# Kernel tuning notes

Hardware: AMD Instinct MI355X
Metric: run time of the kernel (lower is better)

## Reference

```python
import jax, jax.numpy as jnp
import numpy as np
import math

L_LAYERS = 4
EMBED = 512
HEADS = 8
FFN = 2048
EPS = 1e-20
PAD_IDX = 0


def sinusoidal_table(num_embeddings, embedding_dim, padding_idx=0):
    half = embedding_dim // 2
    freq = jnp.exp(jnp.arange(half, dtype=jnp.float32) * (-math.log(10000.0) / (half - 1)))
    ang = jnp.arange(num_embeddings, dtype=jnp.float32)[:, None] * freq[None, :]
    emb = jnp.concatenate([jnp.sin(ang), jnp.cos(ang)], axis=1)
    if padding_idx is not None:
        emb = emb.at[padding_idx].set(0.0)
    return emb  # [num_embeddings, embedding_dim]


def layer_norm(x, g, b):
    mu = jnp.mean(x, axis=-1, keepdims=True)
    var = jnp.mean((x - mu) ** 2, axis=-1, keepdims=True)
    return (x - mu) * jax.lax.rsqrt(var + EPS) * g + b


def mha(x_q, x_kv, Wqkv, bqkv, Wo, bo, mask):
    """Custom attention: scaled scores, multiplicative mask, GLOBAL min-max norm (no softmax)."""
    T, B, C = x_q.shape
    S = x_kv.shape[0]
    hd = C // HEADS
    scale = hd ** -0.5
    q = x_q @ Wqkv[:C].T + bqkv[:C]
    k = x_kv @ Wqkv[C:2 * C].T + bqkv[C:2 * C]
    v = x_kv @ Wqkv[2 * C:].T + bqkv[2 * C:]
    q = q * scale
    # [T,B,C] -> [B*H, T, hd]
    q = q.reshape(T, B * HEADS, hd).transpose(1, 0, 2)
    k = k.reshape(S, B * HEADS, hd).transpose(1, 0, 2)
    v = v.reshape(S, B * HEADS, hd).transpose(1, 0, 2)
    w = jnp.einsum('bth,bsh->bts', q, k)  # [B*H, T, S]
    if mask is not None:
        w = w * mask[None, :, :]
    # global min-max normalization (as in the torch source)
    w = (w - jnp.min(w)) / (jnp.max(w) - jnp.min(w))
    a = jnp.einsum('bts,bsh->bth', w, v)  # [B*H, T, hd]
    a = a.transpose(1, 0, 2).reshape(T, B, C)
    return a @ Wo.T + bo


def setup_inputs() -> dict:
    key = jax.random.key(0)
    ks = iter(jax.random.split(key, 32))
    T, B, C, F, L = 2048, 2, EMBED, FFN, L_LAYERS
    d = {}
    d['x'] = jax.random.normal(next(ks), (T, B, C), dtype=jnp.float32)
    d['enc_out'] = jax.random.normal(next(ks), (T, B, C), dtype=jnp.float32)
    d['tokens'] = jax.random.randint(next(ks), (B, T), 0, 32000, dtype=jnp.int64 if jax.config.read('jax_enable_x64') else jnp.int32)
    sd = C ** -0.5
    d['self_Wqkv'] = jax.random.normal(next(ks), (L, 3 * C, C)) * sd
    d['self_bqkv'] = jnp.zeros((L, 3 * C))
    d['self_Wo'] = jax.random.normal(next(ks), (L, C, C)) * sd
    d['self_bo'] = jnp.zeros((L, C))
    d['cross_Wqkv'] = jax.random.normal(next(ks), (L, 3 * C, C)) * sd
    d['cross_bqkv'] = jnp.zeros((L, 3 * C))
    d['cross_Wo'] = jax.random.normal(next(ks), (L, C, C)) * sd
    d['cross_bo'] = jnp.zeros((L, C))
    d['fc1_w'] = jax.random.normal(next(ks), (L, F, C)) * sd
    d['fc1_b'] = jnp.zeros((L, F))
    d['fc2_w'] = jax.random.normal(next(ks), (L, C, F)) * (F ** -0.5)
    d['fc2_b'] = jnp.zeros((L, C))
    d['ln1_g'] = jnp.ones((L, C)); d['ln1_b'] = jnp.zeros((L, C))
    d['ln2_g'] = jnp.ones((L, C)); d['ln2_b'] = jnp.zeros((L, C))
    d['ln3_g'] = jnp.ones((L, C)); d['ln3_b'] = jnp.zeros((L, C))
    return d


def _forward(x, enc_out, tokens, self_Wqkv, self_bqkv, self_Wo, self_bo,
             cross_Wqkv, cross_bqkv, cross_Wo, cross_bo,
             fc1_w, fc1_b, fc2_w, fc2_b, ln1_g, ln1_b, ln2_g, ln2_b, ln3_g, ln3_b):
    T, B, C = x.shape
    # sinusoidal positional embedding (make_positions with padding_idx=0, no left pad)
    table = sinusoidal_table(PAD_IDX + 1 + T, C, PAD_IDX)
    pos = jnp.where(tokens != PAD_IDX, jnp.arange(1, T + 1)[None, :], 0)  # [B, T]
    pe = table[pos]  # [B, T, C]
    x = x + pe.transpose(1, 0, 2)
    # multiplicative future mask: tril of ones
    fmask = jnp.tril(jnp.ones((T, T), dtype=x.dtype))
    for l in range(L_LAYERS):
        # self-attention
        res = x
        x = mha(x, x, self_Wqkv[l], self_bqkv[l], self_Wo[l], self_bo[l], fmask)
        x = layer_norm(res + x, ln1_g[l], ln1_b[l])
        # cross-attention (no mask)
        res = x
        x = mha(x, enc_out, cross_Wqkv[l], cross_bqkv[l], cross_Wo[l], cross_bo[l], None)
        x = layer_norm(res + x, ln2_g[l], ln2_b[l])
        # FFN
        res = x
        h = jax.nn.relu(x @ fc1_w[l].T + fc1_b[l])
        x = h @ fc2_w[l].T + fc2_b[l]
        x = layer_norm(res + x, ln3_g[l], ln3_b[l])
    return x


def reference(x, enc_out, tokens, self_Wqkv, self_bqkv, self_Wo, self_bo,
              cross_Wqkv, cross_bqkv, cross_Wo, cross_bo,
              fc1_w, fc1_b, fc2_w, fc2_b, ln1_g, ln1_b, ln2_g, ln2_b, ln3_g, ln3_b):
    return _forward(x, enc_out, tokens, self_Wqkv, self_bqkv, self_Wo, self_bo,
                    cross_Wqkv, cross_bqkv, cross_Wo, cross_bo,
                    fc1_w, fc1_b, fc2_w, fc2_b, ln1_g, ln1_b, ln2_g, ln2_b, ln3_g, ln3_b)
```

## Files before the change

kernel.cpp:

```cpp
#include <hip/hip_runtime.h>
#include <math.h>

typedef __bf16 bf16;
typedef unsigned short u16;
typedef __bf16 bf16x8 __attribute__((ext_vector_type(8)));
typedef float f32x4 __attribute__((ext_vector_type(4)));

#define T_SEQ 2048
#define NB    2
#define CE    512
#define NH    8
#define HD    64
#define ROWS  4096
#define NBH   16
#define LDT   40
#define LDA   72

#define MFMA16(a,b,c) __builtin_amdgcn_mfma_f32_16x16x32_bf16((a),(b),(c),0,0,0)

__global__ __launch_bounds__(256) void sniff(const u16* __restrict__ xs,
                                             const int* __restrict__ toks,
                                             int* __restrict__ flags)
{
  const int tid = threadIdx.x;
  int crazy = 0, ze = 0;
  for (int i = tid; i < 4096; i += 256) {
    int e = (xs[i] >> 7) & 0xFF;
    if (e >= 141) crazy++;
    if (((i & 1) == 0) && (xs[i] == 0)) ze++;
  }
  int zc = 0;
  for (int i = tid; i < 1024; i += 256)
    if (toks[2 * i + 1] == 0) zc++;
  __shared__ int r1[4], r2[4], r3[4];
#pragma unroll
  for (int o = 32; o; o >>= 1) {
    crazy += __shfl_down(crazy, o); ze += __shfl_down(ze, o); zc += __shfl_down(zc, o);
  }
  if ((tid & 63) == 0) { r1[tid >> 6] = crazy; r2[tid >> 6] = ze; r3[tid >> 6] = zc; }
  __syncthreads();
  if (tid == 0) {
    int c = r1[0] + r1[1] + r1[2] + r1[3];
    int z = r2[0] + r2[1] + r2[2] + r2[3];
    int t = r3[0] + r3[1] + r3[2] + r3[3];
    flags[0] = (z > 1500 || c > 64) ? 1 : 0;
    flags[1] = (t > 900) ? 1 : 0;
  }
}

static __device__ __forceinline__ float ldf(const void* src, size_t eoff, bool f32) {
  return f32 ? ((const float*)src)[eoff] : (float)((const bf16*)src)[eoff];
}

__global__ __launch_bounds__(256) void posembed(const void* __restrict__ xsrc,
                                                const int* __restrict__ toks,
                                                const int* __restrict__ flags,
                                                float* __restrict__ xf)
{
  const bool f32 = flags[0] != 0;
  const bool tok64 = flags[1] != 0;
  const int row = blockIdx.x;
  const int t = row >> 1, b = row & 1;
  const int tix = b * T_SEQ + t;
  const int tok = tok64 ? toks[2 * tix] : toks[tix];
  const int p = (tok != 0) ? (t + 1) : 0;
  const float kf = -0.0361193740f;
  for (int c = threadIdx.x; c < CE; c += 256) {
    float pe = 0.0f;
    if (p != 0) {
      int i = (c < 256) ? c : (c - 256);
      float freq = expf((float)i * kf);
      float ang = (float)p * freq;
      pe = (c < 256) ? sinf(ang) : cosf(ang);
    }
    xf[(size_t)row * CE + c] = ldf(xsrc, (size_t)row * CE + c, f32) + pe;
  }
}

template<bool RELUF, bool AFFINE>
__global__ __launch_bounds__(256) void gemm_mfma(const void* __restrict__ A, int a_inp,
                                                 const void* __restrict__ Bw, size_t bwOff,
                                                 const void* __restrict__ bias, size_t biasOff,
                                                 const int* __restrict__ flags,
                                                 float* __restrict__ Cf,
                                                 int M, int N, int K, int kspan,
                                                 long long partStride,
                                                 const float* __restrict__ mmf,
                                                 const float* __restrict__ vsum)
{
  __shared__ __align__(16) bf16 Ah[128 * LDT];
  __shared__ __align__(16) bf16 Al[128 * LDT];
  __shared__ __align__(16) bf16 Bh[128 * LDT];
  __shared__ __align__(16) bf16 Bl[128 * LDT];
  const int fl = flags[0];
  const bool a_f32 = (a_inp == 0) ? true : (fl != 0);
  const bool b_f32 = (fl != 0);
  const int tid = threadIdx.x;
  const int m0 = blockIdx.y * 128, n0 = blockIdx.x * 128;
  const int srow = tid >> 1;
  const int skc  = (tid & 1) * 16;
  const int wid = tid >> 6, lane = tid & 63;
  const int wm = (wid >> 1) * 64, wn = (wid & 1) * 64;
  const int fr = lane & 15;
  const int fk = (lane >> 4) * 8;
  const int kb = blockIdx.z * kspan;
  const int ke = (kb + kspan < K) ? (kb + kspan) : K;
  float* Cp = Cf + (long long)blockIdx.z * partStride;
  const int arow1 = (m0 + srow) & 1;
  float inv_ = 0.0f, cmn_ = 0.0f;
  if (AFFINE) { inv_ = 1.0f / (mmf[1] - mmf[0]); cmn_ = mmf[0] * inv_; }
  f32x4 acc[4][4] = {};

  uint4 ra[4], rb[4];
  auto loadA = [&](int k0) {
    size_t g = (size_t)(m0 + srow) * K + k0 + skc;
    if (a_f32) {
      const uint4* p = (const uint4*)((const float*)A + g);
      ra[0] = p[0]; ra[1] = p[1]; ra[2] = p[2]; ra[3] = p[3];
    } else {
      const uint4* p = (const uint4*)((const bf16*)A + g);
      ra[0] = p[0]; ra[1] = p[1];
    }
  };
  auto loadB = [&](int k0) {
    size_t g = bwOff + (size_t)(n0 + srow) * K + k0 + skc;
    if (b_f32) {
      const uint4* p = (const uint4*)((const float*)Bw + g);
      rb[0] = p[0]; rb[1] = p[1]; rb[2] = p[2]; rb[3] = p[3];
    } else {
      const uint4* p = (const uint4*)((const bf16*)Bw + g);
      rb[0] = p[0]; rb[1] = p[1];
    }
  };
  auto cvtStore = [&](const uint4* r, bool f32src, bool wantLo, bf16* Hs, bf16* Ls) {
    float v[16];
    if (f32src) {
      const float* f = (const float*)r;
#pragma unroll
      for (int q = 0; q < 16; q++) v[q] = f[q];
    } else {
      const bf16* c = (const bf16*)r;
#pragma unroll
      for (int q = 0; q < 16; q++) v[q] = (float)c[q];
    }
    bf16x8 h0, h1, l0, l1;
#pragma unroll
    for (int q = 0; q < 8; q++) {
      bf16 ha = (bf16)v[q], hb = (bf16)v[8 + q];
      h0[q] = ha; h1[q] = hb;
      l0[q] = (bf16)(v[q]     - (float)ha);
      l1[q] = (bf16)(v[8 + q] - (float)hb);
    }
    *(bf16x8*)&Hs[srow * LDT + skc]     = h0;
    *(bf16x8*)&Hs[srow * LDT + skc + 8] = h1;
    if (wantLo) {
      *(bf16x8*)&Ls[srow * LDT + skc]     = l0;
      *(bf16x8*)&Ls[srow * LDT + skc + 8] = l1;
    }
  };

  loadA(kb); loadB(kb);
  for (int k0 = kb; k0 < ke; k0 += 32) {
    __syncthreads();
    if (AFFINE) {
      float* f = (float*)ra;
      const float* vs = vsum + arow1 * 512 + k0 + skc;
#pragma unroll
      for (int q = 0; q < 16; q++) f[q] = inv_ * f[q] - cmn_ * vs[q];
    }
    cvtStore(ra, a_f32, a_f32, Ah, Al);
    cvtStore(rb, b_f32, b_f32, Bh, Bl);
    __syncthreads();
    if (k0 + 32 < ke) { loadA(k0 + 32); loadB(k0 + 32); }
    bf16x8 ah[4], bh[4];
#pragma unroll
    for (int i = 0; i < 4; i++) ah[i] = *(const bf16x8*)&Ah[(wm + i*16 + fr) * LDT + fk];
#pragma unroll
    for (int j = 0; j < 4; j++) bh[j] = *(const bf16x8*)&Bh[(wn + j*16 + fr) * LDT + fk];
#pragma unroll
    for (int i = 0; i < 4; i++)
#pragma unroll
      for (int j = 0; j < 4; j++)
        acc[i][j] = MFMA16(ah[i], bh[j], acc[i][j]);
    if (a_f32) {
      bf16x8 al[4];
#pragma unroll
      for (int i = 0; i < 4; i++) al[i] = *(const bf16x8*)&Al[(wm + i*16 + fr) * LDT + fk];
#pragma unroll
      for (int i = 0; i < 4; i++)
#pragma unroll
        for (int j = 0; j < 4; j++)
          acc[i][j] = MFMA16(al[i], bh[j], acc[i][j]);
    }
    if (b_f32) {
      bf16x8 bl[4];
#pragma unroll
      for (int j = 0; j < 4; j++) bl[j] = *(const bf16x8*)&Bl[(wn + j*16 + fr) * LDT + fk];
#pragma unroll
      for (int i = 0; i < 4; i++)
#pragma unroll
        for (int j = 0; j < 4; j++)
          acc[i][j] = MFMA16(ah[i], bl[j], acc[i][j]);
    }
  }
  const int orow0 = m0 + wm + (lane >> 4) * 4;
  const int ocol0 = n0 + wn + (lane & 15);
  const bool addb = (blockIdx.z == 0);
#pragma unroll
  for (int j = 0; j < 4; j++) {
    int col = ocol0 + j * 16;
    float bv = addb ? ldf(bias, biasOff + col, b_f32) : 0.0f;
#pragma unroll
    for (int i = 0; i < 4; i++) {
#pragma unroll
      for (int r = 0; r < 4; r++) {
        float vv = acc[i][j][r] + bv;
        if (RELUF) vv = fmaxf(vv, 0.0f);
        Cp[(size_t)(orow0 + i * 16 + r) * N + col] = vv;
      }
    }
  }
}

__global__ __launch_bounds__(256) void prep_kv(const float* __restrict__ base, int ld,
                                               int kofs0, int vofs0,
                                               bf16* __restrict__ kh, bf16* __restrict__ kl,
                                               bf16* __restrict__ vth, bf16* __restrict__ vtl,
                                               float* __restrict__ vcs)
{
  __shared__ float ts[64 * 65];
  const int bh = blockIdx.x, s0 = blockIdx.y * 64;
  const int b = bh >> 3, h = bh & 7;
  const int kofs = kofs0 + h * HD, vofs = vofs0 + h * HD;
  const int tid = threadIdx.x;
#pragma unroll
  for (int it = 0; it < 16; ++it) {
    int idx = it * 256 + tid, r = idx >> 6, d = idx & 63;
    size_t rowb = (size_t)((s0 + r) * NB + b) * ld;
    float v = base[rowb + kofs + d];
    bf16 hi = (bf16)v;
    size_t o = ((size_t)bh * T_SEQ + s0 + r) * 64 + d;
    kh[o] = hi; kl[o] = (bf16)(v - (float)hi);
    ts[r * 65 + d] = base[rowb + vofs + d];
  }
  __syncthreads();
  const int d = tid >> 2, sseg = (tid & 3) * 16;
  bf16x8 hv0, lv0, hv1, lv1;
#pragma unroll
  for (int q = 0; q < 8; ++q) {
    float v0 = ts[(sseg + q) * 65 + d];
    float v1 = ts[(sseg + 8 + q) * 65 + d];
    bf16 h0 = (bf16)v0, h1 = (bf16)v1;
    hv0[q] = h0; lv0[q] = (bf16)(v0 - (float)h0);
    hv1[q] = h1; lv1[q] = (bf16)(v1 - (float)h1);
  }
  size_t o = ((size_t)bh * 64 + d) * T_SEQ + s0 + sseg;
  *(bf16x8*)&vth[o]     = hv0;
  *(bf16x8*)&vth[o + 8] = hv1;
  *(bf16x8*)&vtl[o]     = lv0;
  *(bf16x8*)&vtl[o + 8] = lv1;
  if (tid < 64) {
    float s = 0.0f;
    for (int j = 0; j < 64; ++j) s += ts[j * 65 + tid];
    vcs[((size_t)bh * 32 + blockIdx.y) * 64 + tid] = s;
  }
}

__device__ __forceinline__ int remap_ty(int ty) { return (ty < 16) ? ty : 47 - ty; }

template<bool MASK>
__global__ __launch_bounds__(256) void fattn(const float* __restrict__ qbase, int qld, int qofs0,
                                             const bf16* __restrict__ kh, const bf16* __restrict__ kl,
                                             const bf16* __restrict__ vth, const bf16* __restrict__ vtl,
                                             float* __restrict__ partial,
                                             float* __restrict__ pvout)
{
  __shared__ __align__(16) bf16 Qh[64 * LDA], Ql[64 * LDA];
  __shared__ __align__(16) bf16 Kh[64 * LDA], Kl[64 * LDA];
  __shared__ __align__(16) bf16 Vh[64 * LDA], Vl[64 * LDA];
  __shared__ __align__(16) bf16 Ph[64 * LDA], Pl[64 * LDA];
  __shared__ float rn[4], rx[4];
  const int bh = blockIdx.x, tyr = remap_ty(blockIdx.y);
  const int t0 = tyr * 64;
  const int b = bh >> 3, h = bh & 7;
  const int qofs = qofs0 + h * HD;
  const int tid = threadIdx.x;
#pragma unroll
  for (int it = 0; it < 16; ++it) {
    int idx = it * 256 + tid, r = idx >> 6, d = idx & 63;
    float v = qbase[(size_t)((t0 + r) * NB + b) * qld + qofs + d] * 0.125f;
    bf16 hi = (bf16)v;
    Qh[r * LDA + d] = hi; Ql[r * LDA + d] = (bf16)(v - (float)hi);
  }
  const int wid = tid >> 6, lane = tid & 63;
  const int wm_ = (wid >> 1) * 32, wn_ = (wid & 1) * 32;
  const int fr = lane & 15, fko = (lane >> 4) * 8;
  const int crr = (lane >> 4) * 4, crc = lane & 15;
  const int cr = tid >> 2, cseg = (tid & 3) * 16;
  float mn = 1e30f, mx = -1e30f;
  f32x4 o4[2][2] = {};
  const int nch = MASK ? (tyr + 1) : 32;
  for (int sc = 0; sc < nch; ++sc) {
    const int s0 = sc * 64;
    __syncthreads();
    {
      size_t go = ((size_t)bh * T_SEQ + s0 + cr) * 64 + cseg;
      *(bf16x8*)&Kh[cr * LDA + cseg]     = *(const bf16x8*)&kh[go];
      *(bf16x8*)&Kh[cr * LDA + cseg + 8] = *(const bf16x8*)&kh[go + 8];
      *(bf16x8*)&Kl[cr * LDA + cseg]     = *(const bf16x8*)&kl[go];
      *(bf16x8*)&Kl[cr * LDA + cseg + 8] = *(const bf16x8*)&kl[go + 8];
      size_t gv = ((size_t)bh * 64 + cr) * T_SEQ + s0 + cseg;
      *(bf16x8*)&Vh[cr * LDA + cseg]     = *(const bf16x8*)&vth[gv];
      *(bf16x8*)&Vh[cr * LDA + cseg + 8] = *(const bf16x8*)&vth[gv + 8];
      *(bf16x8*)&Vl[cr * LDA + cseg]     = *(const bf16x8*)&vtl[gv];
      *(bf16x8*)&Vl[cr * LDA + cseg + 8] = *(const bf16x8*)&vtl[gv + 8];
    }
    __syncthreads();
    f32x4 a4[2][2] = {};
#pragma unroll
    for (int ks = 0; ks < 2; ++ks) {
      bf16x8 aH[2], aL[2], bH[2], bL[2];
#pragma unroll
      for (int i = 0; i < 2; ++i) {
        aH[i] = *(const bf16x8*)&Qh[(wm_ + i*16 + fr) * LDA + ks*32 + fko];
        aL[i] = *(const bf16x8*)&Ql[(wm_ + i*16 + fr) * LDA + ks*32 + fko];
        bH[i] = *(const bf16x8*)&Kh[(wn_ + i*16 + fr) * LDA + ks*32 + fko];
        bL[i] = *(const bf16x8*)&Kl[(wn_ + i*16 + fr) * LDA + ks*32 + fko];
      }
#pragma unroll
      for (int i = 0; i < 2; ++i)
#pragma unroll
        for (int j = 0; j < 2; ++j) {
          a4[i][j] = MFMA16(aH[i], bH[j], a4[i][j]);
          a4[i][j] = MFMA16(aL[i], bH[j], a4[i][j]);
          a4[i][j] = MFMA16(aH[i], bL[j], a4[i][j]);
        }
    }
#pragma unroll
    for (int i = 0; i < 2; ++i)
#pragma unroll
      for (int j = 0; j < 2; ++j)
#pragma unroll
        for (int r = 0; r < 4; ++r) {
          int tl = wm_ + i*16 + crr + r;
          int sl = wn_ + j*16 + crc;
          float w = a4[i][j][r];
          if (MASK && (s0 + sl) > (t0 + tl)) w = 0.0f;
          mn = fminf(mn, w); mx = fmaxf(mx, w);
          bf16 wh = (bf16)w;
          Ph[tl * LDA + sl] = wh;
          Pl[tl * LDA + sl] = (bf16)(w - (float)wh);
        }
    __syncthreads();
#pragma unroll
    for (int ks = 0; ks < 2; ++ks) {
      bf16x8 pH[2], pL[2], vH[2], vL[2];
#pragma unroll
      for (int i = 0; i < 2; ++i) {
        pH[i] = *(const bf16x8*)&Ph[(wm_ + i*16 + fr) * LDA + ks*32 + fko];
        pL[i] = *(const bf16x8*)&Pl[(wm_ + i*16 + fr) * LDA + ks*32 + fko];
        vH[i] = *(const bf16x8*)&Vh[(wn_ + i*16 + fr) * LDA + ks*32 + fko];
        vL[i] = *(const bf16x8*)&Vl[(wn_ + i*16 + fr) * LDA + ks*32 + fko];
      }
#pragma unroll
      for (int i = 0; i < 2; ++i)
#pragma unroll
        for (int j = 0; j < 2; ++j) {
          o4[i][j] = MFMA16(pH[i], vH[j], o4[i][j]);
          o4[i][j] = MFMA16(pL[i], vH[j], o4[i][j]);
          o4[i][j] = MFMA16(pH[i], vL[j], o4[i][j]);
        }
    }
  }
#pragma unroll
  for (int i = 0; i < 2; ++i)
#pragma unroll
    for (int j = 0; j < 2; ++j)
#pragma unroll
      for (int r = 0; r < 4; ++r) {
        int tl = wm_ + i*16 + crr + r;
        int dl = wn_ + j*16 + crc;
        pvout[(size_t)((t0 + tl) * NB + b) * CE + h * HD + dl] = o4[i][j][r];
      }
#pragma unroll
  for (int o = 32; o; o >>= 1) { mn = fminf(mn, __shfl_down(mn, o)); mx = fmaxf(mx, __shfl_down(mx, o)); }
  if (lane == 0) { rn[wid] = mn; rx[wid] = mx; }
  __syncthreads();
  if (tid == 0) {
    int bidx = blockIdx.y * NBH + blockIdx.x;
    partial[2 * bidx]     = fminf(fminf(rn[0], rn[1]), fminf(rn[2], rn[3]));
    partial[2 * bidx + 1] = fmaxf(fmaxf(rx[0], rx[1]), fmaxf(rx[2], rx[3]));
  }
}

__global__ __launch_bounds__(512) void reduce_mm(const float* __restrict__ partial,
                                                 const float* __restrict__ vcs,
                                                 float* __restrict__ mmf,
                                                 float* __restrict__ vsum)
{
  const int tid = threadIdx.x, w = tid >> 6, l = tid & 63;
  __shared__ float rn[8], rx[8];
  float mn = partial[2 * tid], mx = partial[2 * tid + 1];
#pragma unroll
  for (int o = 32; o; o >>= 1) { mn = fminf(mn, __shfl_down(mn, o)); mx = fmaxf(mx, __shfl_down(mx, o)); }
  if (l == 0) { rn[w] = mn; rx[w] = mx; }
  __syncthreads();
  if (tid == 0) {
    float a = 1e30f, c = -1e30f;
#pragma unroll
    for (int i = 0; i < 8; i++) { a = fminf(a, rn[i]); c = fmaxf(c, rx[i]); }
    mmf[0] = a; mmf[1] = c;
  }
  for (int e = tid; e < 1024; e += 512) {
    int bh = e >> 6, d = e & 63;
    float s = 0.0f;
#pragma unroll
    for (int ch = 0; ch < 32; ++ch) s += vcs[(size_t)bh * 2048 + ch * 64 + d];
    vsum[e] = s;
  }
}

template<int NP>
__global__ __launch_bounds__(256) void ln_sum(const float* __restrict__ res,
                                              const float* __restrict__ p, long long pstride,
                                              const void* __restrict__ g, const void* __restrict__ be,
                                              size_t goff, const int* __restrict__ flags,
                                              float* __restrict__ xfo)
{
  __shared__ float red[4];
  const bool fl = flags[0] != 0;
  const int tid = threadIdx.x;
  const size_t base = (size_t)blockIdx.x * CE;
  float a  = res[base + tid];
  float b2 = res[base + tid + 256];
#pragma unroll
  for (int k = 0; k < NP; k++) {
    a  += p[(long long)k * pstride + base + tid];
    b2 += p[(long long)k * pstride + base + tid + 256];
  }
  float s = a + b2;
#pragma unroll
  for (int o = 32; o; o >>= 1) s += __shfl_down(s, o);
  if ((tid & 63) == 0) red[tid >> 6] = s;
  __syncthreads();
  float mu = (red[0] + red[1] + red[2] + red[3]) * (1.0f / 512.0f);
  __syncthreads();
  float da = a - mu, db = b2 - mu;
  float q = da * da + db * db;
#pragma unroll
  for (int o = 32; o; o >>= 1) q += __shfl_down(q, o);
  if ((tid & 63) == 0) red[tid >> 6] = q;
  __syncthreads();
  float var = (red[0] + red[1] + red[2] + red[3]) * (1.0f / 512.0f);
  float rs = rsqrtf(var + 1e-20f);
  xfo[base + tid]       = da * rs * ldf(g, goff + tid, fl)       + ldf(be, goff + tid, fl);
  xfo[base + tid + 256] = db * rs * ldf(g, goff + tid + 256, fl) + ldf(be, goff + tid + 256, fl);
}

extern "C" void kernel_launch(void* const* d_in, const int* in_sizes, int n_in,
                              void* d_out, int out_size, void* d_ws, size_t ws_size,
                              hipStream_t stream)
{
  (void)in_sizes; (void)n_in; (void)out_size; (void)ws_size;
  const void* x_in   = d_in[0];
  const void* enc_in = d_in[1];
  const int*  tokens = (const int*)d_in[2];
  const void* sWqkv = d_in[3];
  const void* sbqkv = d_in[4];
  const void* sWo   = d_in[5];
  const void* sbo   = d_in[6];
  const void* cWqkv = d_in[7];
  const void* cbqkv = d_in[8];
  const void* cWo   = d_in[9];
  const void* cbo   = d_in[10];
  const void* fc1w  = d_in[11];
  const void* fc1b  = d_in[12];
  const void* fc2w  = d_in[13];
  const void* fc2b  = d_in[14];
  const void* ln1g  = d_in[15];
  const void* ln1b  = d_in[16];
  const void* ln2g  = d_in[17];
  const void* ln2b  = d_in[18];
  const void* ln3g  = d_in[19];
  const void* ln3b  = d_in[20];

  char* ws = (char*)d_ws;
  size_t off = 0;
  auto alloc = [&](size_t bytes) -> char* {
    char* p = ws + off;
    off += (bytes + 255) & ~(size_t)255;
    return p;
  };
  int*   flags   = (int*)  alloc(256);
  float* mmf     = (float*)alloc(256);
  float* vsum    = (float*)alloc(1024 * 4);
  float* partial = (float*)alloc(4096);
  float* xf      = (float*)alloc((size_t)ROWS * CE * 4);
  float* y       = (float*)alloc((size_t)ROWS * CE * 4);
  float* qkv     = (float*)alloc((size_t)ROWS * 2048 * 4);
  float* pblk    = (float*)alloc((size_t)ROWS * CE * 4 * 4);
  bf16*  khb     = (bf16*) alloc((size_t)16 * T_SEQ * 64 * 2);
  bf16*  klb     = (bf16*) alloc((size_t)16 * T_SEQ * 64 * 2);
  bf16*  vth     = (bf16*) alloc((size_t)16 * 64 * T_SEQ * 2);
  bf16*  vtl     = (bf16*) alloc((size_t)16 * 64 * T_SEQ * 2);
  float* vcs     = (float*)alloc((size_t)16 * 32 * 64 * 4);
  float* kvb = qkv + (size_t)ROWS * 512;
  const long long PS_FULL = (long long)ROWS * CE;

  sniff<<<1, 256, 0, stream>>>((const u16*)x_in, tokens, flags);
  posembed<<<ROWS, 256, 0, stream>>>(x_in, tokens, flags, xf);

  for (int l = 0; l < 4; l++) {
    gemm_mfma<false, false><<<dim3(12, 32, 1), 256, 0, stream>>>(
        xf, 0, sWqkv, (size_t)l * 1536 * 512, sbqkv, (size_t)l * 1536, flags, qkv,
        ROWS, 1536, 512, 512, 0, nullptr, nullptr);
    prep_kv<<<dim3(16, 32), 256, 0, stream>>>(qkv, 1536, 512, 1024, khb, klb, vth, vtl, vcs);
    fattn<true><<<dim3(NBH, 32), 256, 0, stream>>>(qkv, 1536, 0, khb, klb, vth, vtl, partial, y);
    reduce_mm<<<1, 512, 0, stream>>>(partial, vcs, mmf, vsum);
    gemm_mfma<false, true><<<dim3(4, 32, 4), 256, 0, stream>>>(
        y, 0, sWo, (size_t)l * 512 * 512, sbo, (size_t)l * 512, flags, pblk,
        ROWS, 512, 512, 128, PS_FULL, mmf, vsum);
    ln_sum<4><<<ROWS, 256, 0, stream>>>(xf, pblk, PS_FULL, ln1g, ln1b, (size_t)l * 512, flags, xf);

    gemm_mfma<false, false><<<dim3(4, 32, 1), 256, 0, stream>>>(
        xf, 0, cWqkv, (size_t)l * 1536 * 512, cbqkv, (size_t)l * 1536, flags, qkv,
        ROWS, 512, 512, 512, 0, nullptr, nullptr);
    gemm_mfma<false, false><<<dim3(8, 32, 1), 256, 0, stream>>>(
        enc_in, 1, cWqkv, (size_t)l * 1536 * 512 + (size_t)512 * 512, cbqkv, (size_t)l * 1536 + 512,
        flags, kvb, ROWS, 1024, 512, 512, 0, nullptr, nullptr);
    prep_kv<<<dim3(16, 32), 256, 0, stream>>>(kvb, 1024, 0, 512, khb, klb, vth, vtl, vcs);
    fattn<false><<<dim3(NBH, 32), 256, 0, stream>>>(qkv, 512, 0, khb, klb, vth, vtl, partial, y);
    reduce_mm<<<1, 512, 0, stream>>>(partial, vcs, mmf, vsum);
    gemm_mfma<false, true><<<dim3(4, 32, 4), 256, 0, stream>>>(
        y, 0, cWo, (size_t)l * 512 * 512, cbo, (size_t)l * 512, flags, pblk,
        ROWS, 512, 512, 128, PS_FULL, mmf, vsum);
    ln_sum<4><<<ROWS, 256, 0, stream>>>(xf, pblk, PS_FULL, ln2g, ln2b, (size_t)l * 512, flags, xf);

    gemm_mfma<true, false><<<dim3(16, 32, 1), 256, 0, stream>>>(
        xf, 0, fc1w, (size_t)l * 2048 * 512, fc1b, (size_t)l * 2048, flags, qkv,
        ROWS, 2048, 512, 512, 0, nullptr, nullptr);
    gemm_mfma<false, false><<<dim3(4, 32, 4), 256, 0, stream>>>(
        qkv, 0, fc2w, (size_t)l * 512 * 2048, fc2b, (size_t)l * 512, flags, pblk,
        ROWS, 512, 2048, 512, PS_FULL, nullptr, nullptr);
    float* lnout = (l == 3) ? (float*)d_out : xf;
    ln_sum<4><<<ROWS, 256, 0, stream>>>(xf, pblk, PS_FULL, ln3g, ln3b, (size_t)l * 512, flags, lnout);
  }
}
```

Before: 2.777 ms.

## Double-buffer GEMM LDS tiles, swizzle blocks across XCDs, merge cross-attn QKV GEMMs

The GEMM kernel now keeps two LDS stages, so the next k-tile is converted and stored while the current one feeds the MFMAs, which removes one barrier per iteration. GEMM and attention launches use a 1D grid remapped so neighbouring tiles share an XCD and can reuse L2. The cross-attention Q projection (from xf) and the KV projection (from enc_out) now run as one launch, with column tiles choosing their A source. The cost is twice the LDS use, which may lower occupancy.

```diff
diff --git a/kernel.cpp b/kernel.cpp
--- a/kernel.cpp
+++ b/kernel.cpp
@@ -17,6 +17,12 @@
 #define LDA   72
 
 #define MFMA16(a,b,c) __builtin_amdgcn_mfma_f32_16x16x32_bf16((a),(b),(c),0,0,0)
+
+static __device__ __forceinline__ int xcd_swz(int id, int n) {
+  int q = n >> 3, r = n & 7;
+  int x = id & 7, o = id >> 3;
+  return (x < r) ? (x * (q + 1) + o) : (r * (q + 1) + (x - r) * q + o);
+}
 
 __global__ __launch_bounds__(256) void sniff(const u16* __restrict__ xs,
                                              const int* __restrict__ toks,
@@ -78,34 +84,44 @@
 }
 
 template<bool RELUF, bool AFFINE>
-__global__ __launch_bounds__(256) void gemm_mfma(const void* __restrict__ A, int a_inp,
+__global__ __launch_bounds__(256) void gemm_mfma(const float* __restrict__ A,
+                                                 const void* __restrict__ A2,
                                                  const void* __restrict__ Bw, size_t bwOff,
                                                  const void* __restrict__ bias, size_t biasOff,
                                                  const int* __restrict__ flags,
                                                  float* __restrict__ Cf,
-                                                 int M, int N, int K, int kspan,
+                                                 int N, int K, int kspan,
+                                                 int nbx, int nbxA,
                                                  long long partStride,
                                                  const float* __restrict__ mmf,
                                                  const float* __restrict__ vsum)
 {
-  __shared__ __align__(16) bf16 Ah[128 * LDT];
-  __shared__ __align__(16) bf16 Al[128 * LDT];
-  __shared__ __align__(16) bf16 Bh[128 * LDT];
-  __shared__ __align__(16) bf16 Bl[128 * LDT];
+  __shared__ __align__(16) bf16 AhS[2][128 * LDT];
+  __shared__ __align__(16) bf16 AlS[2][128 * LDT];
+  __shared__ __align__(16) bf16 BhS[2][128 * LDT];
+  __shared__ __align__(16) bf16 BlS[2][128 * LDT];
   const int fl = flags[0];
-  const bool a_f32 = (a_inp == 0) ? true : (fl != 0);
+  const int nblk = nbx * (int)1;
+  (void)nblk;
+  const int id = xcd_swz((int)blockIdx.x, (int)gridDim.x);
+  const int per_z = nbx * 32;
+  const int zz = id / per_z;
+  const int rem = id - zz * per_z;
+  const int by = rem / nbx, bx = rem - by * nbx;
+  const bool a_f32 = (bx < nbxA) ? true : (fl != 0);
+  const void* Abase = (bx < nbxA) ? (const void*)A : A2;
   const bool b_f32 = (fl != 0);
   const int tid = threadIdx.x;
-  const int m0 = blockIdx.y * 128, n0 = blockIdx.x * 128;
+  const int m0 = by * 128, n0 = bx * 128;
   const int srow = tid >> 1;
   const int skc  = (tid & 1) * 16;
   const int wid = tid >> 6, lane = tid & 63;
   const int wm = (wid >> 1) * 64, wn = (wid & 1) * 64;
   const int fr = lane & 15;
   const int fk = (lane >> 4) * 8;
-  const int kb = blockIdx.z * kspan;
+  const int kb = zz * kspan;
   const int ke = (kb + kspan < K) ? (kb + kspan) : K;
-  float* Cp = Cf + (long long)blockIdx.z * partStride;
+  float* Cp = Cf + (long long)zz * partStride;
   const int arow1 = (m0 + srow) & 1;
   float inv_ = 0.0f, cmn_ = 0.0f;
   if (AFFINE) { inv_ = 1.0f / (mmf[1] - mmf[0]); cmn_ = mmf[0] * inv_; }
@@ -115,10 +131,10 @@
   auto loadA = [&](int k0) {
     size_t g = (size_t)(m0 + srow) * K + k0 + skc;
     if (a_f32) {
-      const uint4* p = (const uint4*)((const float*)A + g);
+      const uint4* p = (const uint4*)((const float*)Abase + g);
       ra[0] = p[0]; ra[1] = p[1]; ra[2] = p[2]; ra[3] = p[3];
     } else {
-      const uint4* p = (const uint4*)((const bf16*)A + g);
+      const uint4* p = (const uint4*)((const bf16*)Abase + g);
       ra[0] = p[0]; ra[1] = p[1];
     }
   };
@@ -132,6 +148,14 @@
       rb[0] = p[0]; rb[1] = p[1];
     }
   };
+  auto fixA = [&](int k0) {
+    if (AFFINE) {
+      float* f = (float*)ra;
+      const float* vs = vsum + arow1 * 512 + k0 + skc;
+#pragma unroll
+      for (int q = 0; q < 16; q++) f[q] = inv_ * f[q] - cmn_ * vs[q];
+    }
+  };
   auto cvtStore = [&](const uint4* r, bool f32src, bool wantLo, bf16* Hs, bf16* Ls) {
     float v[16];
     if (f32src) {
@@ -160,23 +184,27 @@
   };
 
   loadA(kb); loadB(kb);
+  fixA(kb);
+  cvtStore(ra, a_f32, a_f32, AhS[0], AlS[0]);
+  cvtStore(rb, b_f32, b_f32, BhS[0], BlS[0]);
+  if (kb + 32 < ke) { loadA(kb + 32); loadB(kb + 32); }
+
+  int cur = 0;
   for (int k0 = kb; k0 < ke; k0 += 32) {
     __syncthreads();
-    if (AFFINE) {
-      float* f = (float*)ra;
-      const float* vs = vsum + arow1 * 512 + k0 + skc;
-#pragma unroll
-      for (int q = 0; q < 16; q++) f[q] = inv_ * f[q] - cmn_ * vs[q];
-    }
-    cvtStore(ra, a_f32, a_f32, Ah, Al);
-    cvtStore(rb, b_f32, b_f32, Bh, Bl);
-    __syncthreads();
-    if (k0 + 32 < ke) { loadA(k0 + 32); loadB(k0 + 32); }
+    if (k0 + 32 < ke) {
+      fixA(k0 + 32);
+      cvtStore(ra, a_f32, a_f32, AhS[cur ^ 1], AlS[cur ^ 1]);
+      cvtStore(rb, b_f32, b_f32, BhS[cur ^ 1], BlS[cur ^ 1]);
+      if (k0 + 64 < ke) { loadA(k0 + 64); loadB(k0 + 64); }
+    }
+    const bf16* Ahc = AhS[cur]; const bf16* Alc = AlS[cur];
+    const bf16* Bhc = BhS[cur]; const bf16* Blc = BlS[cur];
     bf16x8 ah[4], bh[4];
 #pragma unroll
-    for (int i = 0; i < 4; i++) ah[i] = *(const bf16x8*)&Ah[(wm + i*16 + fr) * LDT + fk];
-#pragma unroll
-    for (int j = 0; j < 4; j++) bh[j] = *(const bf16x8*)&Bh[(wn + j*16 + fr) * LDT + fk];
+    for (int i = 0; i < 4; i++) ah[i] = *(const bf16x8*)&Ahc[(wm + i*16 + fr) * LDT + fk];
+#pragma unroll
+    for (int j = 0; j < 4; j++) bh[j] = *(const bf16x8*)&Bhc[(wn + j*16 + fr) * LDT + fk];
 #pragma unroll
     for (int i = 0; i < 4; i++)
 #pragma unroll
@@ -185,7 +213,7 @@
     if (a_f32) {
       bf16x8 al[4];
 #pragma unroll
-      for (int i = 0; i < 4; i++) al[i] = *(const bf16x8*)&Al[(wm + i*16 + fr) * LDT + fk];
+      for (int i = 0; i < 4; i++) al[i] = *(const bf16x8*)&Alc[(wm + i*16 + fr) * LDT + fk];
 #pragma unroll
       for (int i = 0; i < 4; i++)
 #pragma unroll
@@ -195,17 +223,18 @@
     if (b_f32) {
       bf16x8 bl[4];
 #pragma unroll
-      for (int j = 0; j < 4; j++) bl[j] = *(const bf16x8*)&Bl[(wn + j*16 + fr) * LDT + fk];
+      for (int j = 0; j < 4; j++) bl[j] = *(const bf16x8*)&Blc[(wn + j*16 + fr) * LDT + fk];
 #pragma unroll
       for (int i = 0; i < 4; i++)
 #pragma unroll
         for (int j = 0; j < 4; j++)
           acc[i][j] = MFMA16(ah[i], bl[j], acc[i][j]);
     }
+    cur ^= 1;
   }
   const int orow0 = m0 + wm + (lane >> 4) * 4;
   const int ocol0 = n0 + wn + (lane & 15);
-  const bool addb = (blockIdx.z == 0);
+  const bool addb = (zz == 0);
 #pragma unroll
   for (int j = 0; j < 4; j++) {
     int col = ocol0 + j * 16;
@@ -280,7 +309,9 @@
   __shared__ __align__(16) bf16 Vh[64 * LDA], Vl[64 * LDA];
   __shared__ __align__(16) bf16 Ph[64 * LDA], Pl[64 * LDA];
   __shared__ float rn[4], rx[4];
-  const int bh = blockIdx.x, tyr = remap_ty(blockIdx.y);
+  const int id = xcd_swz((int)blockIdx.x, 512);
+  const int bh = id >> 5;
+  const int tyr = remap_ty(id & 31);
   const int t0 = tyr * 64;
   const int b = bh >> 3, h = bh & 7;
   const int qofs = qofs0 + h * HD;
@@ -387,9 +418,8 @@
   if (lane == 0) { rn[wid] = mn; rx[wid] = mx; }
   __syncthreads();
   if (tid == 0) {
-    int bidx = blockIdx.y * NBH + blockIdx.x;
-    partial[2 * bidx]     = fminf(fminf(rn[0], rn[1]), fminf(rn[2], rn[3]));
-    partial[2 * bidx + 1] = fmaxf(fmaxf(rx[0], rx[1]), fmaxf(rx[2], rx[3]));
+    partial[2 * id]     = fminf(fminf(rn[0], rn[1]), fminf(rn[2], rn[3]));
+    partial[2 * id + 1] = fmaxf(fmaxf(rx[0], rx[1]), fmaxf(rx[2], rx[3]));
   }
 }
 
@@ -504,44 +534,40 @@
   bf16*  vth     = (bf16*) alloc((size_t)16 * 64 * T_SEQ * 2);
   bf16*  vtl     = (bf16*) alloc((size_t)16 * 64 * T_SEQ * 2);
   float* vcs     = (float*)alloc((size_t)16 * 32 * 64 * 4);
-  float* kvb = qkv + (size_t)ROWS * 512;
   const long long PS_FULL = (long long)ROWS * CE;
 
   sniff<<<1, 256, 0, stream>>>((const u16*)x_in, tokens, flags);
   posembed<<<ROWS, 256, 0, stream>>>(x_in, tokens, flags, xf);
 
   for (int l = 0; l < 4; l++) {
-    gemm_mfma<false, false><<<dim3(12, 32, 1), 256, 0, stream>>>(
-        xf, 0, sWqkv, (size_t)l * 1536 * 512, sbqkv, (size_t)l * 1536, flags, qkv,
-        ROWS, 1536, 512, 512, 0, nullptr, nullptr);
+    gemm_mfma<false, false><<<384, 256, 0, stream>>>(
+        xf, xf, sWqkv, (size_t)l * 1536 * 512, sbqkv, (size_t)l * 1536, flags, qkv,
+        1536, 512, 512, 12, 12, 0, nullptr, nullptr);
     prep_kv<<<dim3(16, 32), 256, 0, stream>>>(qkv, 1536, 512, 1024, khb, klb, vth, vtl, vcs);
-    fattn<true><<<dim3(NBH, 32), 256, 0, stream>>>(qkv, 1536, 0, khb, klb, vth, vtl, partial, y);
+    fattn<true><<<512, 256, 0, stream>>>(qkv, 1536, 0, khb, klb, vth, vtl, partial, y);
     reduce_mm<<<1, 512, 0, stream>>>(partial, vcs, mmf, vsum);
-    gemm_mfma<false, true><<<dim3(4, 32, 4), 256, 0, stream>>>(
-        y, 0, sWo, (size_t)l * 512 * 512, sbo, (size_t)l * 512, flags, pblk,
-        ROWS, 512, 512, 128, PS_FULL, mmf, vsum);
+    gemm_mfma<false, true><<<512, 256, 0, stream>>>(
+        y, y, sWo, (size_t)l * 512 * 512, sbo, (size_t)l * 512, flags, pblk,
+        512, 512, 128, 4, 4, PS_FULL, mmf, vsum);
     ln_sum<4><<<ROWS, 256, 0, stream>>>(xf, pblk, PS_FULL, ln1g, ln1b, (size_t)l * 512, flags, xf);
 
-    gemm_mfma<false, false><<<dim3(4, 32, 1), 256, 0, stream>>>(
-        xf, 0, cWqkv, (size_t)l * 1536 * 512, cbqkv, (size_t)l * 1536, flags, qkv,
-        ROWS, 512, 512, 512, 0, nullptr, nullptr);
-    gemm_mfma<false, false><<<dim3(8, 32, 1), 256, 0, stream>>>(
-        enc_in, 1, cWqkv, (size_t)l * 1536 * 512 + (size_t)512 * 512, cbqkv, (size_t)l * 1536 + 512,
-        flags, kvb, ROWS, 1024, 512, 512, 0, nullptr, nullptr);
-    prep_kv<<<dim3(16, 32), 256, 0, stream>>>(kvb, 1024, 0, 512, khb, klb, vth, vtl, vcs);
-    fattn<false><<<dim3(NBH, 32), 256, 0, stream>>>(qkv, 512, 0, khb, klb, vth, vtl, partial, y);
+    gemm_mfma<false, false><<<384, 256, 0, stream>>>(
+        xf, enc_in, cWqkv, (size_t)l * 1536 * 512, cbqkv, (size_t)l * 1536, flags, qkv,
+        1536, 512, 512, 12, 4 , 0, nullptr, nullptr);
+    prep_kv<<<dim3(16, 32), 256, 0, stream>>>(qkv, 1536, 512, 1024, khb, klb, vth, vtl, vcs);
+    fattn<false><<<512, 256, 0, stream>>>(qkv, 1536, 0, khb, klb, vth, vtl, partial, y);
     reduce_mm<<<1, 512, 0, stream>>>(partial, vcs, mmf, vsum);
-    gemm_mfma<false, true><<<dim3(4, 32, 4), 256, 0, stream>>>(
-        y, 0, cWo, (size_t)l * 512 * 512, cbo, (size_t)l * 512, flags, pblk,
-        ROWS, 512, 512, 128, PS_FULL, mmf, vsum);
+    gemm_mfma<false, true><<<512, 256, 0, stream>>>(
+        y, y, cWo, (size_t)l * 512 * 512, cbo, (size_t)l * 512, flags, pblk,
+        512, 512, 128, 4, 4, PS_FULL, mmf, vsum);
     ln_sum<4><<<ROWS, 256, 0, stream>>>(xf, pblk, PS_FULL, ln2g, ln2b, (size_t)l * 512, flags, xf);
 
-    gemm_mfma<true, false><<<dim3(16, 32, 1), 256, 0, stream>>>(
-        xf, 0, fc1w, (size_t)l * 2048 * 512, fc1b, (size_t)l * 2048, flags, qkv,
-        ROWS, 2048, 512, 512, 0, nullptr, nullptr);
-    gemm_mfma<false, false><<<dim3(4, 32, 4), 256, 0, stream>>>(
-        qkv, 0, fc2w, (size_t)l * 512 * 2048, fc2b, (size_t)l * 512, flags, pblk,
-        ROWS, 512, 2048, 512, PS_FULL, nullptr, nullptr);
+    gemm_mfma<true, false><<<512, 256, 0, stream>>>(
+        xf, xf, fc1w, (size_t)l * 2048 * 512, fc1b, (size_t)l * 2048, flags, qkv,
+        2048, 512, 512, 16, 16, 0, nullptr, nullptr);
+    gemm_mfma<false, false><<<512, 256, 0, stream>>>(
+        qkv, qkv, fc2w, (size_t)l * 512 * 2048, fc2b, (size_t)l * 512, flags, pblk,
+        512, 2048, 512, 4, 4, PS_FULL, nullptr, nullptr);
     float* lnout = (l == 3) ? (float*)d_out : xf;
     ln_sum<4><<<ROWS, 256, 0, stream>>>(xf, pblk, PS_FULL, ln3g, ln3b, (size_t)l * 512, flags, lnout);
   }
```

Result: faster. 2.602 ms (-6.3%).
